# Performance work log

Measured on AMD Instinct MI355X. Metric: run time of the kernel, lower is better.

The kernel has to match this reference:

```python
import jax, jax.numpy as jnp
import numpy as np

D_MODEL = 1024
N_HEADS = 16
D_K = D_MODEL // N_HEADS


def setup_inputs() -> dict:
    key = jax.random.key(0)
    ks = jax.random.split(key, 12)
    B, S = 2, 2048
    scale = 1.0 / np.sqrt(D_MODEL)
    inp = {
        "q": jax.random.normal(ks[0], (B, S, D_MODEL), jnp.float32),
        "k": jax.random.normal(ks[1], (B, S, D_MODEL), jnp.float32),
        "v": jax.random.normal(ks[2], (B, S, D_MODEL), jnp.float32),
        "Wq": jax.random.normal(ks[3], (D_MODEL, D_MODEL), jnp.float32) * scale,
        "bq": jnp.zeros((D_MODEL,), jnp.float32),
        "Wk": jax.random.normal(ks[4], (D_MODEL, D_MODEL), jnp.float32) * scale,
        "bk": jnp.zeros((D_MODEL,), jnp.float32),
        "Wv": jax.random.normal(ks[5], (D_MODEL, D_MODEL), jnp.float32) * scale,
        "bv": jnp.zeros((D_MODEL,), jnp.float32),
        "Wo": jax.random.normal(ks[6], (D_MODEL, D_MODEL), jnp.float32) * scale,
        "bo": jnp.zeros((D_MODEL,), jnp.float32),
    }
    return inp


def reference(q, k, v, Wq, bq, Wk, bk, Wv, bv, Wo, bo):
    B, S, _ = q.shape
    # QKV projections, split into heads: [B, H, S, d_k]
    def proj(x, W, b):
        y = x @ W.T + b
        return y.reshape(B, -1, N_HEADS, D_K).transpose(0, 2, 1, 3)

    qh = proj(q, Wq, bq)
    kh = proj(k, Wk, bk)
    vh = proj(v, Wv, bv)

    scores = jnp.einsum("bhqd,bhkd->bhqk", qh, kh) / jnp.sqrt(
        jnp.asarray(D_K, qh.dtype)
    )
    attention = jax.nn.softmax(scores, axis=-1)  # dropout is identity in eval
    out = jnp.einsum("bhqk,bhkd->bhqd", attention, vh)
    out = out.transpose(0, 2, 1, 3).reshape(B, -1, N_HEADS * D_K)
    out = out @ Wo.T + bo
    return (out, attention)
```

## Files before the change

### kernel.cpp

```cpp
#include <hip/hip_runtime.h>

typedef __attribute__((ext_vector_type(4))) float f32x4;
typedef __attribute__((ext_vector_type(4))) unsigned short u16x4;
typedef __attribute__((ext_vector_type(8))) unsigned short u16x8;
typedef __attribute__((ext_vector_type(8))) short short8;
typedef __attribute__((ext_vector_type(4))) unsigned int u32x4;

#define DEVFN static __device__ __forceinline__

DEVFN unsigned short f2bf(float f) {
    union { float f; unsigned int u; } v; v.f = f;
    unsigned int r = v.u + 0x7FFFu + ((v.u >> 16) & 1u);
    return (unsigned short)(r >> 16);
}

DEVFN f32x4 mfma16(short8 a, short8 b, f32x4 c) {
    return __builtin_amdgcn_mfma_f32_16x16x32_bf16(a, b, c, 0, 0, 0);
}


__global__ __launch_bounds__(256) void cvt_w(const float* __restrict__ s,
                                             unsigned short* __restrict__ d) {
    int i = (blockIdx.x * 256 + threadIdx.x) * 4;
    f32x4 v = *(const f32x4*)(s + i);
    u16x4 o;
    o[0] = f2bf(v[0]); o[1] = f2bf(v[1]); o[2] = f2bf(v[2]); o[3] = f2bf(v[3]);
    *(u16x4*)(d + i) = o;
}

__global__ __launch_bounds__(256) void qkv_gemm(
    const float* __restrict__ q, const float* __restrict__ k, const float* __restrict__ v,
    const unsigned short* __restrict__ Wqb, const unsigned short* __restrict__ Wkb,
    const unsigned short* __restrict__ Wvb,
    const float* __restrict__ bq, const float* __restrict__ bk, const float* __restrict__ bv,
    unsigned short* __restrict__ qh, unsigned short* __restrict__ kh,
    unsigned short* __restrict__ vt)
{
    constexpr int AS = 40;
    __shared__ __attribute__((aligned(16))) unsigned short Asm[128 * AS];
    __shared__ __attribute__((aligned(16))) unsigned short Bsm[128 * AS];

    const int z = blockIdx.y;
    const float* X = (z == 0) ? q : (z == 1) ? k : v;
    const unsigned short* W = (z == 0) ? Wqb : (z == 1) ? Wkb : Wvb;
    const float* bias = (z == 0) ? bq : (z == 1) ? bk : bv;

    const int bid0 = blockIdx.x;
    const int swz = (bid0 & 7) * 32 + (bid0 >> 3);
    const int bm = swz >> 3, bn = swz & 7;

    const int tid = threadIdx.x;
    const int lane = tid & 63, wid = tid >> 6;
    const int wm = wid >> 1, wn = wid & 1;
    const int lg = lane >> 4, lr = lane & 15;

    f32x4 acc[4][4] = {};

    const float* Xb = X + (size_t)(bm * 128) * 1024;
    const unsigned short* Wb = W + (size_t)(bn * 128) * 1024;
    const int ar = tid >> 3, ac = (tid & 7) * 4;
    const int br = tid >> 2, bc = (tid & 3) * 8;

    for (int kt = 0; kt < 32; ++kt) {
        __syncthreads();
        #pragma unroll
        for (int s4 = 0; s4 < 4; ++s4) {
            int row = s4 * 32 + ar;
            f32x4 xv = *(const f32x4*)(Xb + (size_t)row * 1024 + kt * 32 + ac);
            u16x4 pk;
            pk[0] = f2bf(xv[0]); pk[1] = f2bf(xv[1]);
            pk[2] = f2bf(xv[2]); pk[3] = f2bf(xv[3]);
            *(u16x4*)(&Asm[row * AS + ac]) = pk;
        }
        #pragma unroll
        for (int s2 = 0; s2 < 2; ++s2) {
            int row = s2 * 64 + br;
            *(u16x8*)(&Bsm[row * AS + bc]) =
                *(const u16x8*)(Wb + (size_t)row * 1024 + kt * 32 + bc);
        }
        __syncthreads();

        short8 af[4], bf[4];
        #pragma unroll
        for (int i = 0; i < 4; i++)
            af[i] = *(const short8*)(&Asm[(wm * 64 + i * 16 + lr) * AS + lg * 8]);
        #pragma unroll
        for (int j = 0; j < 4; j++)
            bf[j] = *(const short8*)(&Bsm[(wn * 64 + j * 16 + lr) * AS + lg * 8]);

        if (z != 2) {
            #pragma unroll
            for (int i = 0; i < 4; i++)
                #pragma unroll
                for (int j = 0; j < 4; j++)
                    acc[i][j] = mfma16(af[i], bf[j], acc[i][j]);
        } else {
            #pragma unroll
            for (int i = 0; i < 4; i++)
                #pragma unroll
                for (int j = 0; j < 4; j++)
                    acc[i][j] = mfma16(bf[i], af[j], acc[i][j]);
        }
    }

    if (z != 2) {
        unsigned short* Y = (z == 0) ? qh : kh;
        #pragma unroll
        for (int i = 0; i < 4; i++) {
            int mrow = bm * 128 + wm * 64 + i * 16 + lg * 4;
            #pragma unroll
            for (int j = 0; j < 4; j++) {
                int ncol = bn * 128 + wn * 64 + j * 16 + lr;
                float bb = bias[ncol];
                #pragma unroll
                for (int ii = 0; ii < 4; ii++)
                    Y[(size_t)(mrow + ii) * 1024 + ncol] = f2bf(acc[i][j][ii] + bb);
            }
        }
    } else {
        #pragma unroll
        for (int i = 0; i < 4; i++) {
            int nrow0 = bn * 128 + wn * 64 + i * 16 + lg * 4;
            #pragma unroll
            for (int j = 0; j < 4; j++) {
                int mcol = bm * 128 + wm * 64 + j * 16 + lr;
                int b_ = mcol >> 11, s_ = mcol & 2047;
                #pragma unroll
                for (int ii = 0; ii < 4; ii++) {
                    int nrow = nrow0 + ii;
                    float val = acc[i][j][ii] + bias[nrow];
                    int h_ = nrow >> 6, d_ = nrow & 63;
                    vt[(size_t)((b_ * 16 + h_) * 64 + d_) * 2048 + s_] = f2bf(val);
                }
            }
        }
    }
}

__global__ __launch_bounds__(256) void attn_stats(
    const unsigned short* __restrict__ qh,
    const unsigned short* __restrict__ kh,
    float* __restrict__ Mbuf, float* __restrict__ Linv)
{
    __shared__ float msm[4][16], lsm[4][16];
    const int bid = blockIdx.x;
    const int bh = ((bid & 7) << 2) | (bid >> 9);
    const int qt = (bid >> 3) & 63;
    const int b = bh >> 4, h = bh & 15;
    const int tid = threadIdx.x, wid = tid >> 6, lane = tid & 63;
    const int lg = lane >> 4, lr = lane & 15;
    const int qg = wid >> 1, ks = wid & 1;
    const int qbase = qt * 32 + qg * 16;

    const unsigned short* Qrow = qh + (size_t)(b * 2048 + qbase + lr) * 1024 + h * 64;
    short8 bq0 = *(const short8*)(Qrow + lg * 8);
    short8 bq1 = *(const short8*)(Qrow + 32 + lg * 8);

    const unsigned short* Kbase = kh + (size_t)(b * 2048 + ks * 1024) * 1024 + h * 64;

    float m = -1e30f, l = 0.f;
    #pragma unroll 1
    for (int kt = 0; kt < 16; ++kt) {
        f32x4 sc[4] = {};
        const unsigned short* Kt = Kbase + (size_t)(kt * 64) * 1024;
        #pragma unroll
        for (int c = 0; c < 4; c++) {
            const unsigned short* Kr = Kt + (size_t)(c * 16 + lr) * 1024 + lg * 8;
            sc[c] = mfma16(*(const short8*)(Kr), bq0, sc[c]);
            sc[c] = mfma16(*(const short8*)(Kr + 32), bq1, sc[c]);
        }
        float tmx = sc[0][0];
        #pragma unroll
        for (int c = 0; c < 4; c++)
            #pragma unroll
            for (int i = 0; i < 4; i++)
                tmx = fmaxf(tmx, sc[c][i]);
        tmx *= 0.125f;
        float mnew = fmaxf(m, tmx);
        float e = 0.f;
        #pragma unroll
        for (int c = 0; c < 4; c++)
            #pragma unroll
            for (int i = 0; i < 4; i++)
                e += __expf(sc[c][i] * 0.125f - mnew);
        l = l * __expf(m - mnew) + e;
        m = mnew;
    }
    #pragma unroll
    for (int d = 16; d <= 32; d <<= 1) {
        float mo = __shfl_xor(m, d, 64);
        float lo = __shfl_xor(l, d, 64);
        float mn = fmaxf(m, mo);
        l = l * __expf(m - mn) + lo * __expf(mo - mn);
        m = mn;
    }
    if (lg == 0) { msm[wid][lr] = m; lsm[wid][lr] = l; }
    __syncthreads();
    if (ks == 0 && lg == 0) {
        float mo = msm[wid + 1][lr], lo = lsm[wid + 1][lr];
        float mn = fmaxf(m, mo);
        float L = l * __expf(m - mn) + lo * __expf(mo - mn);
        int qrow = qbase + lr;
        Mbuf[(size_t)bh * 2048 + qrow] = mn;
        Linv[(size_t)bh * 2048 + qrow] = 1.0f / L;
    }
}

__global__ __launch_bounds__(256) void attn_pv(
    const unsigned short* __restrict__ qh,
    const unsigned short* __restrict__ kh,
    const unsigned short* __restrict__ vt,
    const float* __restrict__ Mbuf, const float* __restrict__ Linv,
    float* __restrict__ attn_out, unsigned short* __restrict__ ctx)
{
    __shared__ float Om[2][1024];
    const int bid = blockIdx.x;
    const int bh = ((bid & 7) << 2) | (bid >> 9);
    const int qt = (bid >> 3) & 63;
    const int b = bh >> 4, h = bh & 15;
    const int tid = threadIdx.x, wid = tid >> 6, lane = tid & 63;
    const int lg = lane >> 4, lr = lane & 15;
    const int qg = wid >> 1, ks = wid & 1;
    const int qbase = qt * 32 + qg * 16;

    const unsigned short* Qrow = qh + (size_t)(b * 2048 + qbase + lr) * 1024 + h * 64;
    short8 bq0 = *(const short8*)(Qrow + lg * 8);
    short8 bq1 = *(const short8*)(Qrow + 32 + lg * 8);

    const float m  = Mbuf[(size_t)bh * 2048 + qbase + lr];
    const float il = Linv[(size_t)bh * 2048 + qbase + lr];

    const unsigned short* Kbase = kh + (size_t)(b * 2048 + ks * 1024) * 1024 + h * 64;
    const unsigned short* Vbase = vt + (size_t)(bh * 64) * 2048 + ks * 1024;
    float* prow = attn_out + (size_t)(bh * 2048 + qbase + lr) * 2048 + ks * 1024;

    const int a0 = lg & 1;
    const bool bswap = (lg == 1) || (lg == 2);

    f32x4 o[4] = {};
    #pragma unroll 1
    for (int kt = 0; kt < 16; ++kt) {
        f32x4 sc[4] = {};
        const unsigned short* Kt = Kbase + (size_t)(kt * 64) * 1024;
        #pragma unroll
        for (int c = 0; c < 4; c++) {
            const unsigned short* Kr = Kt + (size_t)(c * 16 + lr) * 1024 + lg * 8;
            sc[c] = mfma16(*(const short8*)(Kr), bq0, sc[c]);
            sc[c] = mfma16(*(const short8*)(Kr + 32), bq1, sc[c]);
        }
        float p[4][4];
        #pragma unroll
        for (int c = 0; c < 4; c++)
            #pragma unroll
            for (int i = 0; i < 4; i++)
                p[c][i] = __expf(sc[c][i] * 0.125f - m) * il;

        #pragma unroll
        for (int c = 0; c < 4; c++) {
            f32x4 pv = { p[c][0], p[c][1], p[c][2], p[c][3] };
            __builtin_nontemporal_store(pv,
                (f32x4*)(prow + kt * 64 + c * 16 + lg * 4));
        }

        unsigned int w32[4][2];
        #pragma unroll
        for (int c = 0; c < 4; c++)
            #pragma unroll
            for (int w = 0; w < 2; w++)
                asm("v_cvt_pk_bf16_f32 %0, %1, %2"
                    : "=v"(w32[c][w]) : "v"(p[c][2 * w]), "v"(p[c][2 * w + 1]));

        unsigned int Av[2][2][2];
        #pragma unroll
        for (int t = 0; t < 2; t++)
            #pragma unroll
            for (int w = 0; w < 2; w++) {
                unsigned int keep = a0 ? w32[2 * t + 1][w] : w32[2 * t][w];
                unsigned int snd  = a0 ? w32[2 * t][w]     : w32[2 * t + 1][w];
                unsigned int rcv = __shfl_xor(snd, 16, 64);
                Av[t][0][w] = a0 ? rcv : keep;
                Av[t][1][w] = a0 ? keep : rcv;
            }
        unsigned int F[2][2][2];
        #pragma unroll
        for (int t = 0; t < 2; t++)
            #pragma unroll
            for (int s = 0; s < 2; s++)
                #pragma unroll
                for (int w = 0; w < 2; w++) {
                    unsigned int sw = __shfl_xor(Av[t][s][w], 48, 64);
                    F[t][s][w] = bswap ? sw : Av[t][s][w];
                }
        u32x4 paw0 = { F[0][0][0], F[0][0][1], F[0][1][0], F[0][1][1] };
        u32x4 paw1 = { F[1][0][0], F[1][0][1], F[1][1][0], F[1][1][1] };
        short8 pa0 = *(short8*)&paw0;
        short8 pa1 = *(short8*)&paw1;

        const unsigned short* Vt = Vbase + kt * 64;
        #pragma unroll
        for (int g = 0; g < 4; g++) {
            const unsigned short* Vr = Vt + (size_t)(g * 16 + lr) * 2048 + lg * 8;
            o[g] = mfma16(pa0, *(const short8*)(Vr), o[g]);
            o[g] = mfma16(pa1, *(const short8*)(Vr + 32), o[g]);
        }
    }

    __syncthreads();
    float* Obuf = &Om[qg][0];
    if (ks == 1) {
        #pragma unroll
        for (int g = 0; g < 4; g++)
            #pragma unroll
            for (int i = 0; i < 4; i++)
                Obuf[(lg * 4 + i) * 64 + g * 16 + lr] = o[g][i];
    }
    __syncthreads();
    if (ks == 0) {
        #pragma unroll
        for (int g = 0; g < 4; g++)
            #pragma unroll
            for (int i = 0; i < 4; i++) {
                float val = o[g][i] + Obuf[(lg * 4 + i) * 64 + g * 16 + lr];
                int qrow = qbase + lg * 4 + i;
                int dcol = h * 64 + g * 16 + lr;
                ctx[(size_t)(b * 2048 + qrow) * 1024 + dcol] = f2bf(val);
            }
    }
}

__global__ __launch_bounds__(256) void out_gemm(
    const unsigned short* __restrict__ ctx, const unsigned short* __restrict__ Wob,
    const float* __restrict__ bo, float* __restrict__ out)
{
    constexpr int AS = 40;
    __shared__ __attribute__((aligned(16))) unsigned short Asm[128 * AS];
    __shared__ __attribute__((aligned(16))) unsigned short Bsm[128 * AS];

    const int bid0 = blockIdx.x;
    const int swz = (bid0 & 7) * 32 + (bid0 >> 3);
    const int bm = swz >> 3, bn = swz & 7;
    const int tid = threadIdx.x;
    const int lane = tid & 63, wid = tid >> 6;
    const int wm = wid >> 1, wn = wid & 1;
    const int lg = lane >> 4, lr = lane & 15;

    f32x4 acc[4][4] = {};

    const unsigned short* Ab = ctx + (size_t)(bm * 128) * 1024;
    const unsigned short* Wb = Wob + (size_t)(bn * 128) * 1024;
    const int br = tid >> 2, bc = (tid & 3) * 8;

    for (int kt = 0; kt < 32; ++kt) {
        __syncthreads();
        #pragma unroll
        for (int s2 = 0; s2 < 2; ++s2) {
            int row = s2 * 64 + br;
            *(u16x8*)(&Asm[row * AS + bc]) =
                *(const u16x8*)(Ab + (size_t)row * 1024 + kt * 32 + bc);
            *(u16x8*)(&Bsm[row * AS + bc]) =
                *(const u16x8*)(Wb + (size_t)row * 1024 + kt * 32 + bc);
        }
        __syncthreads();

        short8 af[4], bf[4];
        #pragma unroll
        for (int i = 0; i < 4; i++)
            af[i] = *(const short8*)(&Asm[(wm * 64 + i * 16 + lr) * AS + lg * 8]);
        #pragma unroll
        for (int j = 0; j < 4; j++)
            bf[j] = *(const short8*)(&Bsm[(wn * 64 + j * 16 + lr) * AS + lg * 8]);
        #pragma unroll
        for (int i = 0; i < 4; i++)
            #pragma unroll
            for (int j = 0; j < 4; j++)
                acc[i][j] = mfma16(af[i], bf[j], acc[i][j]);
    }

    #pragma unroll
    for (int i = 0; i < 4; i++) {
        int mrow = bm * 128 + wm * 64 + i * 16 + lg * 4;
        #pragma unroll
        for (int j = 0; j < 4; j++) {
            int ncol = bn * 128 + wn * 64 + j * 16 + lr;
            float bb = bo[ncol];
            #pragma unroll
            for (int ii = 0; ii < 4; ii++)
                out[(size_t)(mrow + ii) * 1024 + ncol] = acc[i][j][ii] + bb;
        }
    }
}

extern "C" void kernel_launch(void* const* d_in, const int* in_sizes, int n_in,
                              void* d_out, int out_size, void* d_ws, size_t ws_size,
                              hipStream_t stream) {
    const float* q  = (const float*)d_in[0];
    const float* k  = (const float*)d_in[1];
    const float* v  = (const float*)d_in[2];
    const float* Wq = (const float*)d_in[3];
    const float* bq = (const float*)d_in[4];
    const float* Wk = (const float*)d_in[5];
    const float* bk = (const float*)d_in[6];
    const float* Wv = (const float*)d_in[7];
    const float* bv = (const float*)d_in[8];
    const float* Wo = (const float*)d_in[9];
    const float* bo = (const float*)d_in[10];

    float* out  = (float*)d_out;
    float* attn = out + (size_t)4096 * 1024;

    unsigned short* wsp = (unsigned short*)d_ws;
    unsigned short* Wqb = wsp;
    unsigned short* Wkb = wsp + (size_t)(1 << 20);
    unsigned short* Wvb = wsp + (size_t)2 * (1 << 20);
    unsigned short* Wob = wsp + (size_t)3 * (1 << 20);
    unsigned short* qh  = wsp + (size_t)4 * (1 << 20);
    unsigned short* kh  = wsp + (size_t)8 * (1 << 20);
    unsigned short* vt  = wsp + (size_t)12 * (1 << 20);
    unsigned short* ctx = wsp + (size_t)16 * (1 << 20);
    float* Mbuf = (float*)(wsp + (size_t)20 * (1 << 20));
    float* Linv = Mbuf + (size_t)32 * 2048;

    cvt_w<<<1024, 256, 0, stream>>>(Wq, Wqb);
    cvt_w<<<1024, 256, 0, stream>>>(Wk, Wkb);
    cvt_w<<<1024, 256, 0, stream>>>(Wv, Wvb);
    cvt_w<<<1024, 256, 0, stream>>>(Wo, Wob);

    qkv_gemm<<<dim3(256, 3), 256, 0, stream>>>(q, k, v, Wqb, Wkb, Wvb,
                                               bq, bk, bv, qh, kh, vt);

    attn_stats<<<2048, 256, 0, stream>>>(qh, kh, Mbuf, Linv);

    attn_pv<<<2048, 256, 0, stream>>>(qh, kh, vt, Mbuf, Linv, attn, ctx);

    out_gemm<<<256, 256, 0, stream>>>(ctx, Wob, bo, out);
}
```

Measured before the change: 476.7 us.

## Fuse attention stats and PV passes into one kernel holding probabilities in registers

Merges the two-pass attention (stats kernel, then recompute QK^T plus PV) into one kernel. Each block now handles 16 query rows, with four waves each splitting the key range into 512-key chunks. Unnormalized exp scores are kept as packed bf16 in registers, the row sum is reduced through shared memory, and then the probabilities are normalized, written out, and used for PV. This removes the second QK^T computation and the second K read, and folds the four weight-conversion launches into one. The trade-offs are that max subtraction is dropped, which risks overflow for large scores, and the stored attention probabilities are now bf16-rounded values. The 64-register paw array per thread also adds register pressure.

After: 417.8 us. 12.4% less time.

```diff
diff --git a/kernel.cpp b/kernel.cpp
--- a/kernel.cpp
+++ b/kernel.cpp
@@ -19,8 +19,14 @@
 }
 
 
-__global__ __launch_bounds__(256) void cvt_w(const float* __restrict__ s,
-                                             unsigned short* __restrict__ d) {
+__global__ __launch_bounds__(256) void cvt_w4(
+    const float* __restrict__ w0, const float* __restrict__ w1,
+    const float* __restrict__ w2, const float* __restrict__ w3,
+    unsigned short* __restrict__ d0, unsigned short* __restrict__ d1,
+    unsigned short* __restrict__ d2, unsigned short* __restrict__ d3) {
+    const int z = blockIdx.y;
+    const float* s = (z == 0) ? w0 : (z == 1) ? w1 : (z == 2) ? w2 : w3;
+    unsigned short* d = (z == 0) ? d0 : (z == 1) ? d1 : (z == 2) ? d2 : d3;
     int i = (blockIdx.x * 256 + threadIdx.x) * 4;
     f32x4 v = *(const f32x4*)(s + i);
     u16x4 o;
@@ -137,30 +143,38 @@
     }
 }
 
-__global__ __launch_bounds__(256) void attn_stats(
+__global__ __launch_bounds__(256) void attn_fused(
     const unsigned short* __restrict__ qh,
     const unsigned short* __restrict__ kh,
-    float* __restrict__ Mbuf, float* __restrict__ Linv)
+    const unsigned short* __restrict__ vt,
+    float* __restrict__ attn_out, unsigned short* __restrict__ ctx)
 {
-    __shared__ float msm[4][16], lsm[4][16];
+    __shared__ float Lsm[4][16];
+    __shared__ float Om[3][1024];
+
     const int bid = blockIdx.x;
-    const int bh = ((bid & 7) << 2) | (bid >> 9);
-    const int qt = (bid >> 3) & 63;
+    const int swz = (bid & 7) * 512 + (bid >> 3);
+    const int bh = swz >> 7, qt = swz & 127;
     const int b = bh >> 4, h = bh & 15;
-    const int tid = threadIdx.x, wid = tid >> 6, lane = tid & 63;
+    const int tid = threadIdx.x, ks = tid >> 6, lane = tid & 63;
     const int lg = lane >> 4, lr = lane & 15;
-    const int qg = wid >> 1, ks = wid & 1;
-    const int qbase = qt * 32 + qg * 16;
+    const int qbase = qt * 16;
 
     const unsigned short* Qrow = qh + (size_t)(b * 2048 + qbase + lr) * 1024 + h * 64;
     short8 bq0 = *(const short8*)(Qrow + lg * 8);
     short8 bq1 = *(const short8*)(Qrow + 32 + lg * 8);
 
-    const unsigned short* Kbase = kh + (size_t)(b * 2048 + ks * 1024) * 1024 + h * 64;
-
-    float m = -1e30f, l = 0.f;
-    #pragma unroll 1
-    for (int kt = 0; kt < 16; ++kt) {
+    const unsigned short* Kbase = kh + (size_t)(b * 2048 + ks * 512) * 1024 + h * 64;
+    const unsigned short* Vbase = vt + (size_t)(bh * 64) * 2048 + ks * 512;
+
+    const int a0 = lg & 1;
+    const bool bswap = (lg == 1) || (lg == 2);
+
+    unsigned int paw[8][8];
+    float lsum = 0.f;
+
+    #pragma unroll
+    for (int kt = 0; kt < 8; ++kt) {
         f32x4 sc[4] = {};
         const unsigned short* Kt = Kbase + (size_t)(kt * 64) * 1024;
         #pragma unroll
@@ -169,98 +183,14 @@
             sc[c] = mfma16(*(const short8*)(Kr), bq0, sc[c]);
             sc[c] = mfma16(*(const short8*)(Kr + 32), bq1, sc[c]);
         }
-        float tmx = sc[0][0];
+        float p[4][4];
         #pragma unroll
         for (int c = 0; c < 4; c++)
             #pragma unroll
-            for (int i = 0; i < 4; i++)
-                tmx = fmaxf(tmx, sc[c][i]);
-        tmx *= 0.125f;
-        float mnew = fmaxf(m, tmx);
-        float e = 0.f;
-        #pragma unroll
-        for (int c = 0; c < 4; c++)
-            #pragma unroll
-            for (int i = 0; i < 4; i++)
-                e += __expf(sc[c][i] * 0.125f - mnew);
-        l = l * __expf(m - mnew) + e;
-        m = mnew;
-    }
-    #pragma unroll
-    for (int d = 16; d <= 32; d <<= 1) {
-        float mo = __shfl_xor(m, d, 64);
-        float lo = __shfl_xor(l, d, 64);
-        float mn = fmaxf(m, mo);
-        l = l * __expf(m - mn) + lo * __expf(mo - mn);
-        m = mn;
-    }
-    if (lg == 0) { msm[wid][lr] = m; lsm[wid][lr] = l; }
-    __syncthreads();
-    if (ks == 0 && lg == 0) {
-        float mo = msm[wid + 1][lr], lo = lsm[wid + 1][lr];
-        float mn = fmaxf(m, mo);
-        float L = l * __expf(m - mn) + lo * __expf(mo - mn);
-        int qrow = qbase + lr;
-        Mbuf[(size_t)bh * 2048 + qrow] = mn;
-        Linv[(size_t)bh * 2048 + qrow] = 1.0f / L;
-    }
-}
-
-__global__ __launch_bounds__(256) void attn_pv(
-    const unsigned short* __restrict__ qh,
-    const unsigned short* __restrict__ kh,
-    const unsigned short* __restrict__ vt,
-    const float* __restrict__ Mbuf, const float* __restrict__ Linv,
-    float* __restrict__ attn_out, unsigned short* __restrict__ ctx)
-{
-    __shared__ float Om[2][1024];
-    const int bid = blockIdx.x;
-    const int bh = ((bid & 7) << 2) | (bid >> 9);
-    const int qt = (bid >> 3) & 63;
-    const int b = bh >> 4, h = bh & 15;
-    const int tid = threadIdx.x, wid = tid >> 6, lane = tid & 63;
-    const int lg = lane >> 4, lr = lane & 15;
-    const int qg = wid >> 1, ks = wid & 1;
-    const int qbase = qt * 32 + qg * 16;
-
-    const unsigned short* Qrow = qh + (size_t)(b * 2048 + qbase + lr) * 1024 + h * 64;
-    short8 bq0 = *(const short8*)(Qrow + lg * 8);
-    short8 bq1 = *(const short8*)(Qrow + 32 + lg * 8);
-
-    const float m  = Mbuf[(size_t)bh * 2048 + qbase + lr];
-    const float il = Linv[(size_t)bh * 2048 + qbase + lr];
-
-    const unsigned short* Kbase = kh + (size_t)(b * 2048 + ks * 1024) * 1024 + h * 64;
-    const unsigned short* Vbase = vt + (size_t)(bh * 64) * 2048 + ks * 1024;
-    float* prow = attn_out + (size_t)(bh * 2048 + qbase + lr) * 2048 + ks * 1024;
-
-    const int a0 = lg & 1;
-    const bool bswap = (lg == 1) || (lg == 2);
-
-    f32x4 o[4] = {};
-    #pragma unroll 1
-    for (int kt = 0; kt < 16; ++kt) {
-        f32x4 sc[4] = {};
-        const unsigned short* Kt = Kbase + (size_t)(kt * 64) * 1024;
-        #pragma unroll
-        for (int c = 0; c < 4; c++) {
-            const unsigned short* Kr = Kt + (size_t)(c * 16 + lr) * 1024 + lg * 8;
-            sc[c] = mfma16(*(const short8*)(Kr), bq0, sc[c]);
-            sc[c] = mfma16(*(const short8*)(Kr + 32), bq1, sc[c]);
-        }
-        float p[4][4];
-        #pragma unroll
-        for (int c = 0; c < 4; c++)
-            #pragma unroll
-            for (int i = 0; i < 4; i++)
-                p[c][i] = __expf(sc[c][i] * 0.125f - m) * il;
-
-        #pragma unroll
-        for (int c = 0; c < 4; c++) {
-            f32x4 pv = { p[c][0], p[c][1], p[c][2], p[c][3] };
-            __builtin_nontemporal_store(pv,
-                (f32x4*)(prow + kt * 64 + c * 16 + lg * 4));
-        }
+            for (int i = 0; i < 4; i++) {
+                p[c][i] = __expf(sc[c][i] * 0.125f);
+                lsum += p[c][i];
+            }
 
         unsigned int w32[4][2];
         #pragma unroll
@@ -281,7 +211,6 @@
                 Av[t][0][w] = a0 ? rcv : keep;
                 Av[t][1][w] = a0 ? keep : rcv;
             }
-        unsigned int F[2][2][2];
         #pragma unroll
         for (int t = 0; t < 2; t++)
             #pragma unroll
@@ -289,12 +218,44 @@
                 #pragma unroll
                 for (int w = 0; w < 2; w++) {
                     unsigned int sw = __shfl_xor(Av[t][s][w], 48, 64);
-                    F[t][s][w] = bswap ? sw : Av[t][s][w];
+                    paw[kt][t * 4 + s * 2 + w] = bswap ? sw : Av[t][s][w];
                 }
-        u32x4 paw0 = { F[0][0][0], F[0][0][1], F[0][1][0], F[0][1][1] };
-        u32x4 paw1 = { F[1][0][0], F[1][0][1], F[1][1][0], F[1][1][1] };
-        short8 pa0 = *(short8*)&paw0;
-        short8 pa1 = *(short8*)&paw1;
+    }
+
+    lsum += __shfl_xor(lsum, 16, 64);
+    lsum += __shfl_xor(lsum, 32, 64);
+    if (lg == 0) Lsm[ks][lr] = lsum;
+    __syncthreads();
+    const float il = 1.0f / (Lsm[0][lr] + Lsm[1][lr] + Lsm[2][lr] + Lsm[3][lr]);
+
+    float* prow = attn_out + (size_t)(bh * 2048 + qbase + lr) * 2048 + ks * 512;
+    f32x4 o[4] = {};
+    #pragma unroll
+    for (int kt = 0; kt < 8; ++kt) {
+        float sl[8], sh[8];
+        unsigned int s32[8];
+        #pragma unroll
+        for (int r = 0; r < 8; r++) {
+            unsigned int u = paw[kt][r];
+            float lo = __uint_as_float(u << 16) * il;
+            float hi = __uint_as_float(u & 0xFFFF0000u) * il;
+            sl[r] = lo; sh[r] = hi;
+            asm("v_cvt_pk_bf16_f32 %0, %1, %2" : "=v"(s32[r]) : "v"(lo), "v"(hi));
+        }
+        float* pk = prow + kt * 64 + lg * 8;
+        f32x4 st0 = { sl[0], sh[0], sl[1], sh[1] };
+        f32x4 st1 = { sl[2], sh[2], sl[3], sh[3] };
+        f32x4 st2 = { sl[4], sh[4], sl[5], sh[5] };
+        f32x4 st3 = { sl[6], sh[6], sl[7], sh[7] };
+        __builtin_nontemporal_store(st0, (f32x4*)(pk));
+        __builtin_nontemporal_store(st1, (f32x4*)(pk + 4));
+        __builtin_nontemporal_store(st2, (f32x4*)(pk + 32));
+        __builtin_nontemporal_store(st3, (f32x4*)(pk + 36));
+
+        u32x4 w0 = { s32[0], s32[1], s32[2], s32[3] };
+        u32x4 w1 = { s32[4], s32[5], s32[6], s32[7] };
+        short8 pa0 = *(short8*)&w0;
+        short8 pa1 = *(short8*)&w1;
 
         const unsigned short* Vt = Vbase + kt * 64;
         #pragma unroll
@@ -306,13 +267,13 @@
     }
 
     __syncthreads();
-    float* Obuf = &Om[qg][0];
-    if (ks == 1) {
+    if (ks != 0) {
+        float* Ob = &Om[ks - 1][0];
         #pragma unroll
         for (int g = 0; g < 4; g++)
             #pragma unroll
             for (int i = 0; i < 4; i++)
-                Obuf[(lg * 4 + i) * 64 + g * 16 + lr] = o[g][i];
+                Ob[(lg * 4 + i) * 64 + g * 16 + lr] = o[g][i];
     }
     __syncthreads();
     if (ks == 0) {
@@ -320,7 +281,8 @@
         for (int g = 0; g < 4; g++)
             #pragma unroll
             for (int i = 0; i < 4; i++) {
-                float val = o[g][i] + Obuf[(lg * 4 + i) * 64 + g * 16 + lr];
+                int idx = (lg * 4 + i) * 64 + g * 16 + lr;
+                float val = o[g][i] + Om[0][idx] + Om[1][idx] + Om[2][idx];
                 int qrow = qbase + lg * 4 + i;
                 int dcol = h * 64 + g * 16 + lr;
                 ctx[(size_t)(b * 2048 + qrow) * 1024 + dcol] = f2bf(val);
@@ -417,20 +379,13 @@
     unsigned short* kh  = wsp + (size_t)8 * (1 << 20);
     unsigned short* vt  = wsp + (size_t)12 * (1 << 20);
     unsigned short* ctx = wsp + (size_t)16 * (1 << 20);
-    float* Mbuf = (float*)(wsp + (size_t)20 * (1 << 20));
-    float* Linv = Mbuf + (size_t)32 * 2048;
-
-    cvt_w<<<1024, 256, 0, stream>>>(Wq, Wqb);
-    cvt_w<<<1024, 256, 0, stream>>>(Wk, Wkb);
-    cvt_w<<<1024, 256, 0, stream>>>(Wv, Wvb);
-    cvt_w<<<1024, 256, 0, stream>>>(Wo, Wob);
+
+    cvt_w4<<<dim3(1024, 4), 256, 0, stream>>>(Wq, Wk, Wv, Wo, Wqb, Wkb, Wvb, Wob);
 
     qkv_gemm<<<dim3(256, 3), 256, 0, stream>>>(q, k, v, Wqb, Wkb, Wvb,
                                                bq, bk, bv, qh, kh, vt);
 
-    attn_stats<<<2048, 256, 0, stream>>>(qh, kh, Mbuf, Linv);
-
-    attn_pv<<<2048, 256, 0, stream>>>(qh, kh, vt, Mbuf, Linv, attn, ctx);
+    attn_fused<<<4096, 256, 0, stream>>>(qh, kh, vt, attn, ctx);
 
     out_gemm<<<256, 256, 0, stream>>>(ctx, Wob, bo, out);
 }
```
